# Kernel tuning notes

Hardware: AMD Instinct MI355X
Metric: run time of the kernel (lower is better)

## Reference

```python
import jax, jax.numpy as jnp
import numpy as np

EMBED_DIM = 1024
NUM_HEADS = 16
HEAD_DIM = EMBED_DIM // NUM_HEADS
B, N = 8, 1024


def setup_inputs() -> dict:
    key = jax.random.key(0)
    k1, k2, k3, k4, k5, k6 = jax.random.split(key, 6)
    scale = 1.0 / np.sqrt(EMBED_DIM)
    return {
        "x": jax.random.normal(k1, (B, N, EMBED_DIM), dtype=jnp.float32),
        "attn_mask": jax.random.normal(k2, (N, N), dtype=jnp.float32) * 0.1,
        "in_proj_weight": jax.random.normal(k3, (3 * EMBED_DIM, EMBED_DIM), dtype=jnp.float32) * scale,
        "in_proj_bias": jax.random.normal(k4, (3 * EMBED_DIM,), dtype=jnp.float32) * 0.02,
        "out_w": jax.random.normal(k5, (EMBED_DIM, EMBED_DIM), dtype=jnp.float32) * scale,
        "out_b": jax.random.normal(k6, (EMBED_DIM,), dtype=jnp.float32) * 0.02,
    }


def reference(x, attn_mask, in_proj_weight, in_proj_bias, out_w, out_b):
    # x: (B, N, C); fused QKV projection as in forward_direct
    Bn, Nn, C = x.shape
    H, D = NUM_HEADS, HEAD_DIM
    qkv = x @ in_proj_weight.T + in_proj_bias            # (B, N, 3C)
    qkv = qkv.reshape(Bn, Nn, 3, H, D).transpose(2, 0, 3, 1, 4)  # (3, B, H, N, D)
    q, k, v = qkv[0], qkv[1], qkv[2]
    q = q / jnp.sqrt(jnp.asarray(D, dtype=q.dtype))
    attn = jnp.einsum("bhnd,bhmd->bhnm", q, k)           # (B, H, N, N) scores
    attn = attn + attn_mask                              # broadcast over (B, H)
    attn = jax.nn.softmax(attn, axis=-1)
    out = jnp.einsum("bhnm,bhmd->bhnd", attn, v)         # (B, H, N, D)
    out = out.transpose(0, 2, 1, 3).reshape(Bn, Nn, C)   # (B, N, C)
    return out @ out_w.T + out_b
```

## Files before the change

kernel.cpp:

```cpp
#include <hip/hip_runtime.h>


typedef __bf16 bf16x8 __attribute__((ext_vector_type(8)));
typedef float f32x4 __attribute__((ext_vector_type(4)));
typedef unsigned short us4v __attribute__((ext_vector_type(4)));

#define MFMA16 __builtin_amdgcn_mfma_f32_16x16x32_bf16

__device__ __forceinline__ unsigned short f2bf(float f) {
    return __builtin_bit_cast(unsigned short, (__bf16)f);
}

__device__ __forceinline__ us4v cvt4(float4 v) {
    us4v r;
    r.x = f2bf(v.x); r.y = f2bf(v.y); r.z = f2bf(v.z); r.w = f2bf(v.w);
    return r;
}

__device__ __forceinline__ void gl16(const unsigned short* g, unsigned short* l) {
    __builtin_amdgcn_global_load_lds(
        (const __attribute__((address_space(1))) unsigned*)g,
        (__attribute__((address_space(3))) unsigned*)l, 16, 0, 0);
}

__global__ __launch_bounds__(256)
void cvt_bf16(const float* __restrict__ src, unsigned short* __restrict__ dst,
              int n4) {
    const int i = blockIdx.x * 256 + threadIdx.x;
    if (i < n4) {
        float4 v = ((const float4*)src)[i];
        ((us4v*)dst)[i] = cvt4(v);
    }
}

__global__ __launch_bounds__(256, 4)
void transpose_v(const unsigned short* __restrict__ vb,
                 unsigned short* __restrict__ vbT) {
    __shared__ unsigned short t[64 * 66];
    const int bh = blockIdx.x >> 4;
    const int n0 = (blockIdx.x & 15) * 64;
    const int tid = threadIdx.x;
    const int r = tid >> 3;
    const int c = (tid & 7) * 8;
    const unsigned short* src = vb + (size_t)bh * 65536 + (size_t)(n0 + r) * 64 + c;
#pragma unroll
    for (int p = 0; p < 2; ++p) {
        uint4 v = *(const uint4*)(src + (size_t)p * 32 * 64);
        const unsigned short* s = (const unsigned short*)&v;
#pragma unroll
        for (int j = 0; j < 8; ++j)
            t[(c + j) * 66 + (p * 32 + r)] = s[j];
    }
    __syncthreads();
    const int d = tid >> 3;
    const int nc = (tid & 7) * 8;
    unsigned short* dst = vbT + (size_t)bh * 65536 + (size_t)d * 1024 + n0 + nc;
#pragma unroll
    for (int p = 0; p < 2; ++p) {
        uint4 v;
        unsigned short* s = (unsigned short*)&v;
#pragma unroll
        for (int j = 0; j < 8; ++j)
            s[j] = t[(d + p * 32) * 66 + nc + j];
        *(uint4*)(dst + (size_t)p * 32 * 1024) = v;
    }
}

__global__ __launch_bounds__(256, 3)
void qkv_gemm(const unsigned short* __restrict__ xb,
              const unsigned short* __restrict__ wb,
              const float* __restrict__ bias,
              unsigned short* __restrict__ qb, unsigned short* __restrict__ kb,
              unsigned short* __restrict__ vb)
{
    __shared__ unsigned short lsa[128 * 32];
    __shared__ unsigned short lsb[128 * 32];
    const int tid  = threadIdx.x;
    const int wave = tid >> 6, lane = tid & 63;
    const int quad = lane >> 4, l15 = lane & 15;
    const int m0 = blockIdx.x * 128, n0 = blockIdx.y * 128;
    const int wm = (wave & 1) * 64, wn = (wave >> 1) * 64;

    const int srow = wave * 32 + (lane >> 2);
    const int scol = (lane & 3) * 8;
    const unsigned short* ga = xb + (size_t)(m0 + srow) * 1024 + scol;
    const unsigned short* gb = wb + (size_t)(n0 + srow) * 1024 + scol;
    unsigned short* la0 = &lsa[(wave * 32) * 32];
    unsigned short* la1 = &lsa[(wave * 32 + 16) * 32];
    unsigned short* lb0 = &lsb[(wave * 32) * 32];
    unsigned short* lb1 = &lsb[(wave * 32 + 16) * 32];

    f32x4 acc[4][4];
#pragma unroll
    for (int i = 0; i < 4; ++i)
#pragma unroll
        for (int j = 0; j < 4; ++j) acc[i][j] = (f32x4){0.f, 0.f, 0.f, 0.f};

    for (int kt = 0; kt < 32; ++kt) {
        const int k0 = kt * 32;
        __syncthreads();
        gl16(ga + k0, la0);
        gl16(ga + 16 * 1024 + k0, la1);
        gl16(gb + k0, lb0);
        gl16(gb + 16 * 1024 + k0, lb1);
        __syncthreads();
        bf16x8 af[4], bfr[4];
#pragma unroll
        for (int i = 0; i < 4; ++i)
            af[i] = *(const bf16x8*)&lsa[(wm + i * 16 + l15) * 32 + quad * 8];
#pragma unroll
        for (int j = 0; j < 4; ++j)
            bfr[j] = *(const bf16x8*)&lsb[(wn + j * 16 + l15) * 32 + quad * 8];
#pragma unroll
        for (int i = 0; i < 4; ++i)
#pragma unroll
            for (int j = 0; j < 4; ++j)
                acc[i][j] = MFMA16(af[i], bfr[j], acc[i][j], 0, 0, 0);
    }

    const int which = n0 >> 10;
    unsigned short* __restrict__ dst = (which == 0) ? qb : (which == 1) ? kb : vb;
    const float sc = (which == 0) ? 0.125f : 1.0f;
#pragma unroll
    for (int j = 0; j < 4; ++j) {
        const int n = n0 + wn + j * 16 + l15;
        const int c = n & 1023;
        const int h = c >> 6, d = c & 63;
        const float bv = bias[n];
#pragma unroll
        for (int i = 0; i < 4; ++i)
#pragma unroll
            for (int r = 0; r < 4; ++r) {
                const int m = m0 + wm + i * 16 + quad * 4 + r;
                const int b = m >> 10, s = m & 1023;
                const float v = (acc[i][j][r] + bv) * sc;
                dst[(size_t)((b * 16 + h) * 1024 + s) * 64 + d] = f2bf(v);
            }
    }
}

__global__ __launch_bounds__(256, 4)
void attn_kernel(const unsigned short* __restrict__ qb,
                 const unsigned short* __restrict__ kb,
                 const unsigned short* __restrict__ vbT,
                 const float* __restrict__ mask,
                 unsigned short* __restrict__ ob)
{
    __shared__ unsigned short lsk0[64 * 32];
    __shared__ unsigned short lsk1[64 * 32];
    __shared__ unsigned short lsv0[64 * 32];
    __shared__ unsigned short lsv1[64 * 32];
    __shared__ unsigned short lsp[4][16 * 68];
    const int tid  = threadIdx.x;
    const int wave = tid >> 6, lane = tid & 63;
    const int quad = lane >> 4, l15 = lane & 15;
    const int bh = blockIdx.x >> 4;
    const int q0 = (blockIdx.x & 15) * 64;
    const int b = bh >> 4, h = bh & 15;

    const unsigned short* __restrict__ kbase = kb + (size_t)bh * 65536;
    const unsigned short* __restrict__ vtb  = vbT + (size_t)bh * 65536;

    const unsigned short* gk = kbase + (size_t)(wave * 16 + (lane >> 2)) * 64
                                     + (lane & 3) * 8;
    const unsigned short* gv = vtb + (size_t)(wave * 16 + (lane >> 2)) * 1024
                                   + (lane & 3) * 8;
    unsigned short* lk0 = &lsk0[(wave * 16) * 32];
    unsigned short* lk1 = &lsk1[(wave * 16) * 32];
    unsigned short* lv0 = &lsv0[(wave * 16) * 32];
    unsigned short* lv1 = &lsv1[(wave * 16) * 32];

    bf16x8 aq0, aq1;
    {
        const unsigned short* qrow =
            qb + (size_t)(bh * 1024 + q0 + wave * 16 + l15) * 64;
        aq0 = *(const bf16x8*)(qrow + quad * 8);
        aq1 = *(const bf16x8*)(qrow + 32 + quad * 8);
    }

    f32x4 lrun, oacc[4];
#pragma unroll
    for (int r = 0; r < 4; ++r) lrun[r] = 0.f;
#pragma unroll
    for (int nt = 0; nt < 4; ++nt) oacc[nt] = (f32x4){0.f, 0.f, 0.f, 0.f};

    const float* __restrict__ mrow = mask + (size_t)(q0 + wave * 16) * 1024;
    unsigned short* lp = lsp[wave];

    for (int kt = 0; kt < 16; ++kt) {
        __syncthreads();
        gl16(gk + (size_t)kt * 4096, lk0);
        gl16(gk + (size_t)kt * 4096 + 32, lk1);
        gl16(gv + (size_t)kt * 64, lv0);
        gl16(gv + (size_t)kt * 64 + 32, lv1);
        __syncthreads();

        f32x4 s[4];
#pragma unroll
        for (int nt = 0; nt < 4; ++nt) s[nt] = (f32x4){0.f, 0.f, 0.f, 0.f};
#pragma unroll
        for (int nt = 0; nt < 4; ++nt) {
            s[nt] = MFMA16(aq0, *(const bf16x8*)&lsk0[(nt * 16 + l15) * 32 + quad * 8],
                           s[nt], 0, 0, 0);
            s[nt] = MFMA16(aq1, *(const bf16x8*)&lsk1[(nt * 16 + l15) * 32 + quad * 8],
                           s[nt], 0, 0, 0);
        }

#pragma unroll
        for (int nt = 0; nt < 4; ++nt)
#pragma unroll
            for (int r = 0; r < 4; ++r) {
                const float sv = s[nt][r]
                    + mrow[(size_t)(quad * 4 + r) * 1024 + kt * 64 + nt * 16 + l15];
                const float p = __expf(sv);
                lrun[r] += p;
                lp[(quad * 4 + r) * 68 + nt * 16 + l15] = f2bf(p);
            }
        const bf16x8 ap0 = *(const bf16x8*)&lp[l15 * 68 + quad * 8];
        const bf16x8 ap1 = *(const bf16x8*)&lp[l15 * 68 + 32 + quad * 8];

#pragma unroll
        for (int nt = 0; nt < 4; ++nt) {
            oacc[nt] = MFMA16(ap0, *(const bf16x8*)&lsv0[(nt * 16 + l15) * 32 + quad * 8],
                              oacc[nt], 0, 0, 0);
            oacc[nt] = MFMA16(ap1, *(const bf16x8*)&lsv1[(nt * 16 + l15) * 32 + quad * 8],
                              oacc[nt], 0, 0, 0);
        }
    }

#pragma unroll
    for (int off = 1; off < 16; off <<= 1)
#pragma unroll
        for (int r = 0; r < 4; ++r)
            lrun[r] += __shfl_xor(lrun[r], off, 64);

    f32x4 invl;
#pragma unroll
    for (int r = 0; r < 4; ++r) invl[r] = 1.0f / lrun[r];
#pragma unroll
    for (int nt = 0; nt < 4; ++nt)
#pragma unroll
        for (int r = 0; r < 4; ++r) {
            const int srow = q0 + wave * 16 + quad * 4 + r;
            ob[(size_t)(b * 1024 + srow) * 1024 + h * 64 + nt * 16 + l15] =
                f2bf(oacc[nt][r] * invl[r]);
        }
}

__global__ __launch_bounds__(256, 3)
void out_gemm(const unsigned short* __restrict__ a, const float* __restrict__ w,
              const float* __restrict__ bias, float* __restrict__ out)
{
    __shared__ unsigned short lsa[128 * 32];
    __shared__ unsigned short lsb[128 * 32];
    const int tid  = threadIdx.x;
    const int wave = tid >> 6, lane = tid & 63;
    const int quad = lane >> 4, l15 = lane & 15;
    const int m0 = blockIdx.x * 128, n0 = blockIdx.y * 128;
    const int wm = (wave & 1) * 64, wn = (wave >> 1) * 64;
    const int trb = tid >> 3, tcb = tid & 7;

    const int srow = wave * 32 + (lane >> 2);
    const int scol = (lane & 3) * 8;
    const unsigned short* ga = a + (size_t)(m0 + srow) * 1024 + scol;
    unsigned short* la0 = &lsa[(wave * 32) * 32];
    unsigned short* la1 = &lsa[(wave * 32 + 16) * 32];

    f32x4 acc[4][4];
#pragma unroll
    for (int i = 0; i < 4; ++i)
#pragma unroll
        for (int j = 0; j < 4; ++j) acc[i][j] = (f32x4){0.f, 0.f, 0.f, 0.f};

    for (int kt = 0; kt < 32; ++kt) {
        const int k0 = kt * 32;
        float4 fb[4];
#pragma unroll
        for (int i = 0; i < 4; ++i)
            fb[i] = *(const float4*)(w + (size_t)(n0 + i * 32 + trb) * 1024 + k0 + tcb * 4);
        __syncthreads();
        gl16(ga + k0, la0);
        gl16(ga + 16 * 1024 + k0, la1);
#pragma unroll
        for (int i = 0; i < 4; ++i)
            *(us4v*)&lsb[(i * 32 + trb) * 32 + tcb * 4] = cvt4(fb[i]);
        __syncthreads();
        bf16x8 af[4], bfr[4];
#pragma unroll
        for (int i = 0; i < 4; ++i)
            af[i] = *(const bf16x8*)&lsa[(wm + i * 16 + l15) * 32 + quad * 8];
#pragma unroll
        for (int j = 0; j < 4; ++j)
            bfr[j] = *(const bf16x8*)&lsb[(wn + j * 16 + l15) * 32 + quad * 8];
#pragma unroll
        for (int i = 0; i < 4; ++i)
#pragma unroll
            for (int j = 0; j < 4; ++j)
                acc[i][j] = MFMA16(af[i], bfr[j], acc[i][j], 0, 0, 0);
    }

#pragma unroll
    for (int j = 0; j < 4; ++j) {
        const int n = n0 + wn + j * 16 + l15;
        const float bv = bias[n];
#pragma unroll
        for (int i = 0; i < 4; ++i)
#pragma unroll
            for (int r = 0; r < 4; ++r) {
                const int m = m0 + wm + i * 16 + quad * 4 + r;
                out[(size_t)m * 1024 + n] = acc[i][j][r] + bv;
            }
    }
}

extern "C" void kernel_launch(void* const* d_in, const int* in_sizes, int n_in,
                              void* d_out, int out_size, void* d_ws, size_t ws_size,
                              hipStream_t stream) {
    const float* x    = (const float*)d_in[0];
    const float* mask = (const float*)d_in[1];
    const float* win  = (const float*)d_in[2];
    const float* bin  = (const float*)d_in[3];
    const float* wout = (const float*)d_in[4];
    const float* bout = (const float*)d_in[5];
    float* out = (float*)d_out;

    char* ws = (char*)d_ws;
    unsigned short* xb = (unsigned short*)(ws);
    unsigned short* ob = (unsigned short*)(ws);
    unsigned short* qb = (unsigned short*)(ws + (size_t)(16 << 20));
    unsigned short* kb = (unsigned short*)(ws + (size_t)(32 << 20));
    unsigned short* vb = (unsigned short*)(ws + (size_t)(48 << 20));
    unsigned short* winb = (unsigned short*)d_out;
    unsigned short* vbT = (unsigned short*)((char*)d_out + (size_t)(16 << 20));

    cvt_bf16<<<dim3(8192), 256, 0, stream>>>(x, xb, 8 * 1024 * 1024 / 4);
    cvt_bf16<<<dim3(3072), 256, 0, stream>>>(win, winb, 3 * 1024 * 1024 / 4);
    qkv_gemm<<<dim3(64, 24), 256, 0, stream>>>(xb, winb, bin, qb, kb, vb);
    transpose_v<<<dim3(2048), 256, 0, stream>>>(vb, vbT);
    attn_kernel<<<dim3(2048), 256, 0, stream>>>(qb, kb, vbT, mask, ob);
    out_gemm<<<dim3(64, 8), 256, 0, stream>>>(ob, wout, bout, out);
}
```

Measured before the change: 302.7 us.

## Double-buffer K/V tiles in attention kernel and prefetch mask values

The attention kernel now keeps two LDS buffers for each K and V tile. It starts the async global-to-LDS load of the next tile before computing on the current one, which drops one barrier per iteration and hides load latency behind the MFMA work. Mask values for the tile are read into registers before the QK MFMAs, so their global latency overlaps the matrix math. The cost is twice the K/V shared memory, which may lower the number of resident blocks per CU, and extra register pressure from the mask prefetch.

```diff
diff --git a/kernel.cpp b/kernel.cpp
--- a/kernel.cpp
+++ b/kernel.cpp
@@ -146,10 +146,10 @@
                  const float* __restrict__ mask,
                  unsigned short* __restrict__ ob)
 {
-    __shared__ unsigned short lsk0[64 * 32];
-    __shared__ unsigned short lsk1[64 * 32];
-    __shared__ unsigned short lsv0[64 * 32];
-    __shared__ unsigned short lsv1[64 * 32];
+    __shared__ unsigned short lsk0[2][64 * 32];
+    __shared__ unsigned short lsk1[2][64 * 32];
+    __shared__ unsigned short lsv0[2][64 * 32];
+    __shared__ unsigned short lsv1[2][64 * 32];
     __shared__ unsigned short lsp[4][16 * 68];
     const int tid  = threadIdx.x;
     const int wave = tid >> 6, lane = tid & 63;
@@ -165,10 +165,7 @@
                                      + (lane & 3) * 8;
     const unsigned short* gv = vtb + (size_t)(wave * 16 + (lane >> 2)) * 1024
                                    + (lane & 3) * 8;
-    unsigned short* lk0 = &lsk0[(wave * 16) * 32];
-    unsigned short* lk1 = &lsk1[(wave * 16) * 32];
-    unsigned short* lv0 = &lsv0[(wave * 16) * 32];
-    unsigned short* lv1 = &lsv1[(wave * 16) * 32];
+    const int so = (wave * 16) * 32;
 
     bf16x8 aq0, aq1;
     {
@@ -187,32 +184,47 @@
     const float* __restrict__ mrow = mask + (size_t)(q0 + wave * 16) * 1024;
     unsigned short* lp = lsp[wave];
 
+    gl16(gk, &lsk0[0][so]);
+    gl16(gk + 32, &lsk1[0][so]);
+    gl16(gv, &lsv0[0][so]);
+    gl16(gv + 32, &lsv1[0][so]);
+
     for (int kt = 0; kt < 16; ++kt) {
-        __syncthreads();
-        gl16(gk + (size_t)kt * 4096, lk0);
-        gl16(gk + (size_t)kt * 4096 + 32, lk1);
-        gl16(gv + (size_t)kt * 64, lv0);
-        gl16(gv + (size_t)kt * 64 + 32, lv1);
-        __syncthreads();
+        const int cur = kt & 1, nxt = cur ^ 1;
+        __syncthreads();
+        if (kt < 15) {
+            gl16(gk + (size_t)(kt + 1) * 4096, &lsk0[nxt][so]);
+            gl16(gk + (size_t)(kt + 1) * 4096 + 32, &lsk1[nxt][so]);
+            gl16(gv + (size_t)(kt + 1) * 64, &lsv0[nxt][so]);
+            gl16(gv + (size_t)(kt + 1) * 64 + 32, &lsv1[nxt][so]);
+        }
+
+        float mv[4][4];
+#pragma unroll
+        for (int nt = 0; nt < 4; ++nt)
+#pragma unroll
+            for (int r = 0; r < 4; ++r)
+                mv[nt][r] =
+                    mrow[(size_t)(quad * 4 + r) * 1024 + kt * 64 + nt * 16 + l15];
 
         f32x4 s[4];
 #pragma unroll
         for (int nt = 0; nt < 4; ++nt) s[nt] = (f32x4){0.f, 0.f, 0.f, 0.f};
 #pragma unroll
         for (int nt = 0; nt < 4; ++nt) {
-            s[nt] = MFMA16(aq0, *(const bf16x8*)&lsk0[(nt * 16 + l15) * 32 + quad * 8],
-                           s[nt], 0, 0, 0);
-            s[nt] = MFMA16(aq1, *(const bf16x8*)&lsk1[(nt * 16 + l15) * 32 + quad * 8],
-                           s[nt], 0, 0, 0);
+            s[nt] = MFMA16(aq0,
+                *(const bf16x8*)&lsk0[cur][(nt * 16 + l15) * 32 + quad * 8],
+                s[nt], 0, 0, 0);
+            s[nt] = MFMA16(aq1,
+                *(const bf16x8*)&lsk1[cur][(nt * 16 + l15) * 32 + quad * 8],
+                s[nt], 0, 0, 0);
         }
 
 #pragma unroll
         for (int nt = 0; nt < 4; ++nt)
 #pragma unroll
             for (int r = 0; r < 4; ++r) {
-                const float sv = s[nt][r]
-                    + mrow[(size_t)(quad * 4 + r) * 1024 + kt * 64 + nt * 16 + l15];
-                const float p = __expf(sv);
+                const float p = __expf(s[nt][r] + mv[nt][r]);
                 lrun[r] += p;
                 lp[(quad * 4 + r) * 68 + nt * 16 + l15] = f2bf(p);
             }
@@ -221,10 +233,12 @@
 
 #pragma unroll
         for (int nt = 0; nt < 4; ++nt) {
-            oacc[nt] = MFMA16(ap0, *(const bf16x8*)&lsv0[(nt * 16 + l15) * 32 + quad * 8],
-                              oacc[nt], 0, 0, 0);
-            oacc[nt] = MFMA16(ap1, *(const bf16x8*)&lsv1[(nt * 16 + l15) * 32 + quad * 8],
-                              oacc[nt], 0, 0, 0);
+            oacc[nt] = MFMA16(ap0,
+                *(const bf16x8*)&lsv0[cur][(nt * 16 + l15) * 32 + quad * 8],
+                oacc[nt], 0, 0, 0);
+            oacc[nt] = MFMA16(ap1,
+                *(const bf16x8*)&lsv1[cur][(nt * 16 + l15) * 32 + quad * 8],
+                oacc[nt], 0, 0, 0);
         }
     }
 
```

Result: slower. 318.3 us (+5.2%).

## Process two 16-row query tiles per wave in attention kernel

Applied to the files above, without the earlier changes.

Each attention block now covers 128 query rows instead of 64. Each wave handles two 16-row query subtiles against the same K/V tiles staged in shared memory, which halves the grid and the K/V global-to-LDS traffic per query row. The mask loads are also hoisted ahead of the QK MFMAs so their latency can overlap the matrix work. In exchange, register pressure rises (launch bounds lowered from 4 to 2), which can reduce occupancy, and the smaller grid of 1024 blocks gives less parallelism to hide latency.

```diff
diff --git a/kernel.cpp b/kernel.cpp
--- a/kernel.cpp
+++ b/kernel.cpp
@@ -139,7 +139,7 @@
     }
 }
 
-__global__ __launch_bounds__(256, 4)
+__global__ __launch_bounds__(256, 2)
 void attn_kernel(const unsigned short* __restrict__ qb,
                  const unsigned short* __restrict__ kb,
                  const unsigned short* __restrict__ vbT,
@@ -154,8 +154,8 @@
     const int tid  = threadIdx.x;
     const int wave = tid >> 6, lane = tid & 63;
     const int quad = lane >> 4, l15 = lane & 15;
-    const int bh = blockIdx.x >> 4;
-    const int q0 = (blockIdx.x & 15) * 64;
+    const int bh = blockIdx.x >> 3;
+    const int q0 = (blockIdx.x & 7) * 128;
     const int b = bh >> 4, h = bh & 15;
 
     const unsigned short* __restrict__ kbase = kb + (size_t)bh * 65536;
@@ -170,21 +170,24 @@
     unsigned short* lv0 = &lsv0[(wave * 16) * 32];
     unsigned short* lv1 = &lsv1[(wave * 16) * 32];
 
-    bf16x8 aq0, aq1;
-    {
+    bf16x8 aq[2][2];
+#pragma unroll
+    for (int t = 0; t < 2; ++t) {
         const unsigned short* qrow =
-            qb + (size_t)(bh * 1024 + q0 + wave * 16 + l15) * 64;
-        aq0 = *(const bf16x8*)(qrow + quad * 8);
-        aq1 = *(const bf16x8*)(qrow + 32 + quad * 8);
-    }
-
-    f32x4 lrun, oacc[4];
-#pragma unroll
-    for (int r = 0; r < 4; ++r) lrun[r] = 0.f;
-#pragma unroll
-    for (int nt = 0; nt < 4; ++nt) oacc[nt] = (f32x4){0.f, 0.f, 0.f, 0.f};
-
-    const float* __restrict__ mrow = mask + (size_t)(q0 + wave * 16) * 1024;
+            qb + (size_t)(bh * 1024 + q0 + wave * 32 + t * 16 + l15) * 64;
+        aq[t][0] = *(const bf16x8*)(qrow + quad * 8);
+        aq[t][1] = *(const bf16x8*)(qrow + 32 + quad * 8);
+    }
+
+    f32x4 lrun[2], oacc[2][4];
+#pragma unroll
+    for (int t = 0; t < 2; ++t) {
+#pragma unroll
+        for (int r = 0; r < 4; ++r) lrun[t][r] = 0.f;
+#pragma unroll
+        for (int nt = 0; nt < 4; ++nt) oacc[t][nt] = (f32x4){0.f, 0.f, 0.f, 0.f};
+    }
+
     unsigned short* lp = lsp[wave];
 
     for (int kt = 0; kt < 16; ++kt) {
@@ -195,56 +198,73 @@
         gl16(gv + (size_t)kt * 64 + 32, lv1);
         __syncthreads();
 
-        f32x4 s[4];
-#pragma unroll
-        for (int nt = 0; nt < 4; ++nt) s[nt] = (f32x4){0.f, 0.f, 0.f, 0.f};
-#pragma unroll
-        for (int nt = 0; nt < 4; ++nt) {
-            s[nt] = MFMA16(aq0, *(const bf16x8*)&lsk0[(nt * 16 + l15) * 32 + quad * 8],
-                           s[nt], 0, 0, 0);
-            s[nt] = MFMA16(aq1, *(const bf16x8*)&lsk1[(nt * 16 + l15) * 32 + quad * 8],
-                           s[nt], 0, 0, 0);
+#pragma unroll
+        for (int t = 0; t < 2; ++t) {
+            const float* __restrict__ mrow =
+                mask + (size_t)(q0 + wave * 32 + t * 16) * 1024 + kt * 64;
+
+            float mv[4][4];
+#pragma unroll
+            for (int nt = 0; nt < 4; ++nt)
+#pragma unroll
+                for (int r = 0; r < 4; ++r)
+                    mv[nt][r] = mrow[(size_t)(quad * 4 + r) * 1024 + nt * 16 + l15];
+
+            f32x4 s[4];
+#pragma unroll
+            for (int nt = 0; nt < 4; ++nt) s[nt] = (f32x4){0.f, 0.f, 0.f, 0.f};
+#pragma unroll
+            for (int nt = 0; nt < 4; ++nt) {
+                s[nt] = MFMA16(aq[t][0],
+                    *(const bf16x8*)&lsk0[(nt * 16 + l15) * 32 + quad * 8],
+                    s[nt], 0, 0, 0);
+                s[nt] = MFMA16(aq[t][1],
+                    *(const bf16x8*)&lsk1[(nt * 16 + l15) * 32 + quad * 8],
+                    s[nt], 0, 0, 0);
+            }
+
+#pragma unroll
+            for (int nt = 0; nt < 4; ++nt)
+#pragma unroll
+                for (int r = 0; r < 4; ++r) {
+                    const float p = __expf(s[nt][r] + mv[nt][r]);
+                    lrun[t][r] += p;
+                    lp[(quad * 4 + r) * 68 + nt * 16 + l15] = f2bf(p);
+                }
+            const bf16x8 ap0 = *(const bf16x8*)&lp[l15 * 68 + quad * 8];
+            const bf16x8 ap1 = *(const bf16x8*)&lp[l15 * 68 + 32 + quad * 8];
+
+#pragma unroll
+            for (int nt = 0; nt < 4; ++nt) {
+                oacc[t][nt] = MFMA16(ap0,
+                    *(const bf16x8*)&lsv0[(nt * 16 + l15) * 32 + quad * 8],
+                    oacc[t][nt], 0, 0, 0);
+                oacc[t][nt] = MFMA16(ap1,
+                    *(const bf16x8*)&lsv1[(nt * 16 + l15) * 32 + quad * 8],
+                    oacc[t][nt], 0, 0, 0);
+            }
         }
-
+    }
+
+#pragma unroll
+    for (int t = 0; t < 2; ++t) {
+#pragma unroll
+        for (int off = 1; off < 16; off <<= 1)
+#pragma unroll
+            for (int r = 0; r < 4; ++r)
+                lrun[t][r] += __shfl_xor(lrun[t][r], off, 64);
+        f32x4 invl;
+#pragma unroll
+        for (int r = 0; r < 4; ++r) invl[r] = 1.0f / lrun[t][r];
 #pragma unroll
         for (int nt = 0; nt < 4; ++nt)
 #pragma unroll
             for (int r = 0; r < 4; ++r) {
-                const float sv = s[nt][r]
-                    + mrow[(size_t)(quad * 4 + r) * 1024 + kt * 64 + nt * 16 + l15];
-                const float p = __expf(sv);
-                lrun[r] += p;
-                lp[(quad * 4 + r) * 68 + nt * 16 + l15] = f2bf(p);
-            }
-        const bf16x8 ap0 = *(const bf16x8*)&lp[l15 * 68 + quad * 8];
-        const bf16x8 ap1 = *(const bf16x8*)&lp[l15 * 68 + 32 + quad * 8];
-
-#pragma unroll
-        for (int nt = 0; nt < 4; ++nt) {
-            oacc[nt] = MFMA16(ap0, *(const bf16x8*)&lsv0[(nt * 16 + l15) * 32 + quad * 8],
-                              oacc[nt], 0, 0, 0);
-            oacc[nt] = MFMA16(ap1, *(const bf16x8*)&lsv1[(nt * 16 + l15) * 32 + quad * 8],
-                              oacc[nt], 0, 0, 0);
-        }
-    }
-
-#pragma unroll
-    for (int off = 1; off < 16; off <<= 1)
-#pragma unroll
-        for (int r = 0; r < 4; ++r)
-            lrun[r] += __shfl_xor(lrun[r], off, 64);
-
-    f32x4 invl;
-#pragma unroll
-    for (int r = 0; r < 4; ++r) invl[r] = 1.0f / lrun[r];
-#pragma unroll
-    for (int nt = 0; nt < 4; ++nt)
-#pragma unroll
-        for (int r = 0; r < 4; ++r) {
-            const int srow = q0 + wave * 16 + quad * 4 + r;
-            ob[(size_t)(b * 1024 + srow) * 1024 + h * 64 + nt * 16 + l15] =
-                f2bf(oacc[nt][r] * invl[r]);
-        }
+                const int srow = q0 + wave * 32 + t * 16 + quad * 4 + r;
+                ob[(size_t)(b * 1024 + srow) * 1024 + h * 64 + nt * 16 + l15] =
+                    f2bf(oacc[t][nt][r] * invl[r]);
+            }
+    }
 }
 
 __global__ __launch_bounds__(256, 3)
@@ -337,6 +357,6 @@
     cvt_bf16<<<dim3(3072), 256, 0, stream>>>(win, winb, 3 * 1024 * 1024 / 4);
     qkv_gemm<<<dim3(64, 24), 256, 0, stream>>>(xb, winb, bin, qb, kb, vb);
     transpose_v<<<dim3(2048), 256, 0, stream>>>(vb, vbT);
-    attn_kernel<<<dim3(2048), 256, 0, stream>>>(qb, kb, vbT, mask, ob);
+    attn_kernel<<<dim3(1024), 256, 0, stream>>>(qb, kb, vbT, mask, ob);
     out_gemm<<<dim3(64, 8), 256, 0, stream>>>(ob, wout, bout, out);
 }
```

Result: slower. 317.7 us (+5.0%).
